# Kernel optimization log

Measured on AMD Instinct MI355X. Metric: run time of the kernel, lower is better.

Reference implementation:

```python
import jax, jax.numpy as jnp
import numpy as np

B, S, E, H, D = 16, 1024, 768, 12, 64  # batch, seq, n_embd, n_head, head_dim
F = 4 * E
EPS = 1e-5


def layernorm(x, g, b):
    mu = jnp.mean(x, axis=-1, keepdims=True)
    var = jnp.mean((x - mu) ** 2, axis=-1, keepdims=True)
    return (x - mu) * jax.lax.rsqrt(var + EPS) * g + b


def setup_inputs() -> dict:
    key = jax.random.key(0)
    ks = jax.random.split(key, 12)
    w = lambda k, shape: jax.random.normal(k, shape, dtype=jnp.float32) * 0.02
    return {
        "x": jax.random.normal(ks[0], (B, S, E), dtype=jnp.float32),
        # per-head q/k/v projections stacked over heads: [H, E, D]
        "Wq": w(ks[1], (H, E, D)), "bq": jnp.zeros((H, D), jnp.float32),
        "Wk": w(ks[2], (H, E, D)), "bk": jnp.zeros((H, D), jnp.float32),
        "Wv": w(ks[3], (H, E, D)), "bv": jnp.zeros((H, D), jnp.float32),
        "Wp": w(ks[4], (E, E)), "bp": jnp.zeros((E,), jnp.float32),
        "ln1_g": jnp.ones((E,), jnp.float32), "ln1_b": jnp.zeros((E,), jnp.float32),
        "ln2_g": jnp.ones((E,), jnp.float32), "ln2_b": jnp.zeros((E,), jnp.float32),
        "W1": w(ks[5], (E, F)), "b1": jnp.zeros((F,), jnp.float32),
        "W2": w(ks[6], (F, E)), "b2": jnp.zeros((E,), jnp.float32),
        "lnf_g": jnp.ones((E,), jnp.float32), "lnf_b": jnp.zeros((E,), jnp.float32),
    }


def reference(x, Wq, bq, Wk, bk, Wv, bv, Wp, bp,
              ln1_g, ln1_b, ln2_g, ln2_b, W1, b1, W2, b2, lnf_g, lnf_b):
    # --- multi-head causal attention (batched over heads, same math as the
    # per-head loop in the original) ---
    h = layernorm(x, ln1_g, ln1_b)
    q = jnp.einsum('bse,hed->bhsd', h, Wq) + bq[None, :, None, :]
    k = jnp.einsum('bse,hed->bhsd', h, Wk) + bk[None, :, None, :]
    v = jnp.einsum('bse,hed->bhsd', h, Wv) + bv[None, :, None, :]
    scores = jnp.einsum('bhsd,bhtd->bhst', q, k)
    causal = jnp.tril(jnp.ones((S, S), dtype=bool))
    # original: mask with -inf, then divide by sqrt(head_dim), then softmax
    scores = jnp.where(causal, scores, -jnp.inf) / np.sqrt(D).astype(np.float32)
    attn = jax.nn.softmax(scores, axis=-1)
    o = jnp.einsum('bhst,bhtd->bhsd', attn, v)
    o = o.transpose(0, 2, 1, 3).reshape(B, S, E)  # concat heads
    x = x + (o @ Wp + bp)
    # --- FFN with post-net LayerNorm (as in the original FeedForward) ---
    h2 = layernorm(x, ln2_g, ln2_b)
    f = jax.nn.gelu(h2 @ W1 + b1, approximate=False) @ W2 + b2
    f = layernorm(f, lnf_g, lnf_b)
    return x + f
```

## Files before the change

kernel.cpp:

```cpp
#include <hip/hip_runtime.h>
#include <math.h>

typedef unsigned short u16;
typedef __attribute__((ext_vector_type(8))) short s16x8;
typedef __attribute__((ext_vector_type(4))) float f32x4;

#define NB 16
#define NS 1024
#define NE 768
#define NH 12
#define ND 64
#define NF 3072
#define NBS (NB*NS)
#define NBH (NB*NH)

__device__ __forceinline__ u16 f2bf(float f){
  unsigned u = __float_as_uint(f);
  unsigned r = (u + 0x7fffu + ((u >> 16) & 1u)) >> 16;
  return (u16)r;
}

__device__ __forceinline__ void gload16(const void* g, void* l){
  __builtin_amdgcn_global_load_lds((const __attribute__((address_space(1))) void*)g,
                                   (__attribute__((address_space(3))) void*)l, 16, 0, 0);
}

__global__ __launch_bounds__(256) void pack_t(const float* __restrict__ W,
                                              u16* __restrict__ Wt, int N, int K){
  __shared__ u16 tile[64*72];
  const int tid = threadIdx.x;
  const int n0 = blockIdx.x*64, k0 = blockIdx.y*64;
  #pragma unroll
  for (int it = 0; it < 4; ++it){
    int c = it*256 + tid;
    int row = c >> 4, col = (c & 15) * 4;
    float4 v = *(const float4*)(W + (size_t)(k0+row)*N + n0 + col);
    tile[row*72+col+0] = f2bf(v.x); tile[row*72+col+1] = f2bf(v.y);
    tile[row*72+col+2] = f2bf(v.z); tile[row*72+col+3] = f2bf(v.w);
  }
  __syncthreads();
  #pragma unroll
  for (int it = 0; it < 2; ++it){
    int c = it*256 + tid;
    int nr = c >> 3, kc = (c & 7) * 8;
    s16x8 val;
    #pragma unroll
    for (int j = 0; j < 8; ++j) val[j] = tile[(kc+j)*72 + nr];
    *(s16x8*)(Wt + (size_t)(n0+nr)*K + k0 + kc) = val;
  }
}

__global__ __launch_bounds__(256) void pack_qkv(const float* __restrict__ Wq,
    const float* __restrict__ Wk, const float* __restrict__ Wv,
    const float* __restrict__ bq, const float* __restrict__ bk,
    const float* __restrict__ bv, u16* __restrict__ Wt, float* __restrict__ bias){
  __shared__ u16 tile[64*72];
  const int tid = threadIdx.x;
  const int n0 = blockIdx.x*64, e0 = blockIdx.y*64;
  const int p = n0 / NE, rr = n0 % NE, h = rr >> 6;
  const float* Wsrc = (p==0) ? Wq : ((p==1) ? Wk : Wv);
  #pragma unroll
  for (int it = 0; it < 4; ++it){
    int c = it*256 + tid;
    int row = c >> 4, col = (c & 15) * 4;
    float4 v = *(const float4*)(Wsrc + ((size_t)h*NE + e0 + row)*ND + col);
    tile[row*72+col+0] = f2bf(v.x); tile[row*72+col+1] = f2bf(v.y);
    tile[row*72+col+2] = f2bf(v.z); tile[row*72+col+3] = f2bf(v.w);
  }
  __syncthreads();
  #pragma unroll
  for (int it = 0; it < 2; ++it){
    int c = it*256 + tid;
    int dr = c >> 3, ec = (c & 7) * 8;
    s16x8 val;
    #pragma unroll
    for (int j = 0; j < 8; ++j) val[j] = tile[(ec+j)*72 + dr];
    *(s16x8*)(Wt + (size_t)(n0+dr)*NE + e0 + ec) = val;
  }
  if (e0 == 0 && tid < 64){
    const float* bsrc = (p==0) ? bq : ((p==1) ? bk : bv);
    bias[n0 + tid] = bsrc[rr + tid];
  }
}

__global__ __launch_bounds__(256) void ln_bf16(const float* __restrict__ x,
    const float* __restrict__ g, const float* __restrict__ b, u16* __restrict__ out){
  __shared__ float red[4];
  const int row = blockIdx.x, tid = threadIdx.x;
  const float* xr = x + (size_t)row*NE;
  float v0 = xr[tid], v1 = xr[tid+256], v2 = xr[tid+512];
  float s = v0 + v1 + v2;
  #pragma unroll
  for (int off = 32; off > 0; off >>= 1) s += __shfl_down(s, off);
  if ((tid & 63) == 0) red[tid >> 6] = s;
  __syncthreads();
  float mu = (red[0]+red[1]+red[2]+red[3]) * (1.f/NE);
  float d0 = v0-mu, d1 = v1-mu, d2 = v2-mu;
  float q = d0*d0 + d1*d1 + d2*d2;
  #pragma unroll
  for (int off = 32; off > 0; off >>= 1) q += __shfl_down(q, off);
  __syncthreads();
  if ((tid & 63) == 0) red[tid >> 6] = q;
  __syncthreads();
  float rs = rsqrtf((red[0]+red[1]+red[2]+red[3]) * (1.f/NE) + 1e-5f);
  u16* orow = out + (size_t)row*NE;
  orow[tid]     = f2bf(d0*rs*g[tid]     + b[tid]);
  orow[tid+256] = f2bf(d1*rs*g[tid+256] + b[tid+256]);
  orow[tid+512] = f2bf(d2*rs*g[tid+512] + b[tid+512]);
}

__global__ __launch_bounds__(256) void ln_add_out(const float* __restrict__ f2,
    const float* __restrict__ g, const float* __restrict__ b, float* __restrict__ x1){
  __shared__ float red[4];
  const int row = blockIdx.x, tid = threadIdx.x;
  const float* xr = f2 + (size_t)row*NE;
  float v0 = xr[tid], v1 = xr[tid+256], v2 = xr[tid+512];
  float s = v0 + v1 + v2;
  #pragma unroll
  for (int off = 32; off > 0; off >>= 1) s += __shfl_down(s, off);
  if ((tid & 63) == 0) red[tid >> 6] = s;
  __syncthreads();
  float mu = (red[0]+red[1]+red[2]+red[3]) * (1.f/NE);
  float d0 = v0-mu, d1 = v1-mu, d2 = v2-mu;
  float q = d0*d0 + d1*d1 + d2*d2;
  #pragma unroll
  for (int off = 32; off > 0; off >>= 1) q += __shfl_down(q, off);
  __syncthreads();
  if ((tid & 63) == 0) red[tid >> 6] = q;
  __syncthreads();
  float rs = rsqrtf((red[0]+red[1]+red[2]+red[3]) * (1.f/NE) + 1e-5f);
  float* orow = x1 + (size_t)row*NE;
  orow[tid]     += d0*rs*g[tid]     + b[tid];
  orow[tid+256] += d1*rs*g[tid+256] + b[tid+256];
  orow[tid+512] += d2*rs*g[tid+512] + b[tid+512];
}

template<int EPI>
__global__ __launch_bounds__(256, 2)
void gemm_bt(const u16* __restrict__ A, const u16* __restrict__ Bt,
             const float* __restrict__ bias, const float* __restrict__ resid,
             float* __restrict__ outF, u16* __restrict__ outU,
             u16* __restrict__ oq, u16* __restrict__ ok, u16* __restrict__ ov,
             int M, int N, int K)
{
  __shared__ u16 As[128*32];
  __shared__ u16 Bs[128*32];
  const int tid = threadIdx.x;
  const int lane = tid & 63, wv = tid >> 6;
  const int wm = wv >> 1, wn = wv & 1;
  const int r = lane & 15, g4 = lane >> 4;
  const int m0 = blockIdx.y*128, n0 = blockIdx.x*128;

  f32x4 acc[4][4] = {};

  for (int kt = 0; kt < K; kt += 32) {
    __syncthreads();
    #pragma unroll
    for (int it = 0; it < 2; ++it) {
      int c = it*256 + tid;
      int row = c >> 2, kc = (c & 3) << 3;
      gload16(A  + (size_t)(m0+row)*K + kt + kc, As + (size_t)(it*256 + wv*64)*8);
      gload16(Bt + (size_t)(n0+row)*K + kt + kc, Bs + (size_t)(it*256 + wv*64)*8);
    }
    __syncthreads();
    s16x8 aF[4], bF[4];
    #pragma unroll
    for (int mi = 0; mi < 4; ++mi)
      aF[mi] = *(const s16x8*)(As + (wm*64 + mi*16 + r)*32 + g4*8);
    #pragma unroll
    for (int ni = 0; ni < 4; ++ni)
      bF[ni] = *(const s16x8*)(Bs + (wn*64 + ni*16 + r)*32 + g4*8);
    #pragma unroll
    for (int mi = 0; mi < 4; ++mi)
      #pragma unroll
      for (int ni = 0; ni < 4; ++ni)
        acc[mi][ni] = __builtin_amdgcn_mfma_f32_16x16x32_bf16(aF[mi], bF[ni], acc[mi][ni], 0, 0, 0);
  }

  const int colb = n0 + wn*64, rowb = m0 + wm*64;
  #pragma unroll
  for (int mi = 0; mi < 4; ++mi) {
    #pragma unroll
    for (int ni = 0; ni < 4; ++ni) {
      const int col = colb + ni*16 + r;
      const float bv = bias[col];
      #pragma unroll
      for (int i = 0; i < 4; ++i) {
        const int row = rowb + mi*16 + g4*4 + i;
        float v = acc[mi][ni][i] + bv;
        if (EPI == 0) {
          int p = col / NE, rr2 = col % NE;
          int hh = rr2 >> 6, d = rr2 & 63;
          int bb = row >> 10, ss = row & (NS-1);
          size_t idx = (((size_t)(bb*NH + hh))*NS + ss)*ND + d;
          if (p == 1) v *= 0.18033688011112042f;
          u16 val = f2bf(v);
          if (p == 0) oq[idx] = val;
          else if (p == 1) ok[idx] = val;
          else ov[idx] = val;
        } else if (EPI == 1) {
          size_t idx = (size_t)row*NE + col;
          outF[idx] = resid[idx] + v;
        } else if (EPI == 2) {
          float ge = 0.5f * v * (1.0f + erff(v * 0.70710678118654752f));
          outU[(size_t)row*NF + col] = f2bf(ge);
        } else {
          outF[(size_t)row*NE + col] = v;
        }
      }
    }
  }
}

__global__ __launch_bounds__(256) void transpose_v(const u16* __restrict__ v,
                                                   u16* __restrict__ vT){
  __shared__ u16 tile[64*80];
  const int tid = threadIdx.x;
  const int t0 = blockIdx.x*64, bh = blockIdx.y;
  const u16* src = v + ((size_t)bh*NS + t0)*ND;
  #pragma unroll
  for (int it = 0; it < 2; ++it){
    int c = it*256 + tid;
    int row = c >> 3, col = (c & 7) * 8;
    *(s16x8*)(tile + row*80 + col) = *(const s16x8*)(src + (size_t)row*ND + col);
  }
  __syncthreads();
  u16* dst = vT + (size_t)bh*ND*NS + t0;
  #pragma unroll
  for (int it = 0; it < 2; ++it){
    int c = it*256 + tid;
    int d = c >> 3, tc = (c & 7) * 8;
    s16x8 val;
    #pragma unroll
    for (int j = 0; j < 8; ++j) val[j] = tile[(tc+j)*80 + d];
    *(s16x8*)(dst + (size_t)d*NS + tc) = val;
  }
}

__global__ __launch_bounds__(256, 2)
void attn(const u16* __restrict__ q, const u16* __restrict__ k,
          const u16* __restrict__ vT, u16* __restrict__ o)
{
  __shared__ u16 Ks[64*80];
  __shared__ u16 Vs[64*80];
  __shared__ u16 Ps[64*80];
  const int tid = threadIdx.x, lane = tid & 63, w = tid >> 6;
  const int r = lane & 15, g4 = lane >> 4;
  const int phys = blockIdx.y * 8 + blockIdx.x;
  const int logical = (phys & 7) * 192 + (phys >> 3);
  const int bh = logical >> 3, qt = logical & 7;
  const int bb = bh / NH, hh = bh % NH;
  const int rgb0 = qt * 64, rgb1 = (15 - qt) * 64;

  s16x8 qf[2][2];
  {
    const u16* qb = q + ((size_t)bh*NS + w*16 + r)*ND;
    qf[0][0] = *(const s16x8*)(qb + (size_t)rgb0*ND + g4*8);
    qf[0][1] = *(const s16x8*)(qb + (size_t)rgb0*ND + 32 + g4*8);
    qf[1][0] = *(const s16x8*)(qb + (size_t)rgb1*ND + g4*8);
    qf[1][1] = *(const s16x8*)(qb + (size_t)rgb1*ND + 32 + g4*8);
  }

  f32x4 oacc[2][4] = {};
  float mrow[2][4], lrow[2][4];
  #pragma unroll
  for (int rg = 0; rg < 2; ++rg)
    #pragma unroll
    for (int i = 0; i < 4; ++i){ mrow[rg][i] = -INFINITY; lrow[rg][i] = 0.f; }

  const u16* kbase = k  + (size_t)bh*NS*ND;
  const u16* vbase = vT + (size_t)bh*ND*NS;
  const int nt = 16 - qt;

  for (int t = 0; t < nt; ++t) {
    const int kt0 = t*64;
    __syncthreads();
    #pragma unroll
    for (int it = 0; it < 2; ++it) {
      int c = it*256 + tid;
      int rowi = c >> 3, coli = (c & 7) * 8;
      *(s16x8*)(Ks + rowi*80 + coli) = *(const s16x8*)(kbase + (size_t)(kt0+rowi)*ND + coli);
      *(s16x8*)(Vs + rowi*80 + coli) = *(const s16x8*)(vbase + (size_t)rowi*NS + kt0 + coli);
    }
    __syncthreads();

    #pragma unroll
    for (int rg = 0; rg < 2; ++rg) {
      const int rgb = (rg == 0) ? rgb0 : rgb1;
      if (kt0 > rgb) continue;

      f32x4 sc[4];
      __builtin_amdgcn_s_setprio(1);
      #pragma unroll
      for (int ni = 0; ni < 4; ++ni) {
        s16x8 kf0 = *(const s16x8*)(Ks + (ni*16+r)*80 + g4*8);
        s16x8 kf1 = *(const s16x8*)(Ks + (ni*16+r)*80 + 32 + g4*8);
        f32x4 tacc = {};
        tacc = __builtin_amdgcn_mfma_f32_16x16x32_bf16(qf[rg][0], kf0, tacc, 0, 0, 0);
        tacc = __builtin_amdgcn_mfma_f32_16x16x32_bf16(qf[rg][1], kf1, tacc, 0, 0, 0);
        sc[ni] = tacc;
      }
      __builtin_amdgcn_s_setprio(0);

      float mx[4];
      #pragma unroll
      for (int i = 0; i < 4; ++i) mx[i] = mrow[rg][i];
      if (kt0 == rgb) {
        #pragma unroll
        for (int ni = 0; ni < 4; ++ni)
          #pragma unroll
          for (int i = 0; i < 4; ++i) {
            if (ni*16 + r > w*16 + g4*4 + i) sc[ni][i] = -INFINITY;
            mx[i] = fmaxf(mx[i], sc[ni][i]);
          }
      } else {
        #pragma unroll
        for (int ni = 0; ni < 4; ++ni)
          #pragma unroll
          for (int i = 0; i < 4; ++i) mx[i] = fmaxf(mx[i], sc[ni][i]);
      }
      #pragma unroll
      for (int i = 0; i < 4; ++i) {
        #pragma unroll
        for (int off = 1; off < 16; off <<= 1) mx[i] = fmaxf(mx[i], __shfl_xor(mx[i], off));
      }
      bool nogrow = true;
      #pragma unroll
      for (int i = 0; i < 4; ++i) nogrow = nogrow && (mx[i] - mrow[rg][i] <= 8.f);
      float psum[4];
      if (!__all(nogrow)) {
        #pragma unroll
        for (int i = 0; i < 4; ++i) {
          float corr = exp2f(mrow[rg][i] - mx[i]);
          mrow[rg][i] = mx[i];
          lrow[rg][i] *= corr;
          #pragma unroll
          for (int di = 0; di < 4; ++di) oacc[rg][di][i] *= corr;
        }
      }
      #pragma unroll
      for (int ni = 0; ni < 4; ++ni)
        #pragma unroll
        for (int i = 0; i < 4; ++i) {
          float p = exp2f(sc[ni][i] - mrow[rg][i]);
          if (ni == 0) psum[i] = p; else psum[i] += p;
          Ps[(w*16 + g4*4 + i)*80 + ni*16 + r] = f2bf(p);
        }
      #pragma unroll
      for (int i = 0; i < 4; ++i) {
        #pragma unroll
        for (int off = 1; off < 16; off <<= 1) psum[i] += __shfl_xor(psum[i], off);
        lrow[rg][i] += psum[i];
      }
      __builtin_amdgcn_s_setprio(1);
      #pragma unroll
      for (int kk = 0; kk < 2; ++kk) {
        s16x8 pf = *(const s16x8*)(&Ps[(w*16 + r)*80 + kk*32 + g4*8]);
        #pragma unroll
        for (int di = 0; di < 4; ++di) {
          s16x8 vf = *(const s16x8*)(&Vs[(di*16+r)*80 + kk*32 + g4*8]);
          oacc[rg][di] = __builtin_amdgcn_mfma_f32_16x16x32_bf16(pf, vf, oacc[rg][di], 0, 0, 0);
        }
      }
      __builtin_amdgcn_s_setprio(0);
    }
  }

  #pragma unroll
  for (int rg = 0; rg < 2; ++rg) {
    const int rgb = (rg == 0) ? rgb0 : rgb1;
    #pragma unroll
    for (int i = 0; i < 4; ++i) {
      float inv = 1.f / lrow[rg][i];
      int s = rgb + w*16 + g4*4 + i;
      u16* orow = o + ((size_t)(bb*NS + s))*NE + hh*ND;
      #pragma unroll
      for (int di = 0; di < 4; ++di)
        orow[di*16 + r] = f2bf(oacc[rg][di][i] * inv);
    }
  }
}

extern "C" void kernel_launch(void* const* d_in, const int* in_sizes, int n_in,
                              void* d_out, int out_size, void* d_ws, size_t ws_size,
                              hipStream_t stream)
{
  const float* x   = (const float*)d_in[0];
  const float* Wq  = (const float*)d_in[1];
  const float* bq  = (const float*)d_in[2];
  const float* Wk  = (const float*)d_in[3];
  const float* bk  = (const float*)d_in[4];
  const float* Wv  = (const float*)d_in[5];
  const float* bv  = (const float*)d_in[6];
  const float* Wp  = (const float*)d_in[7];
  const float* bp  = (const float*)d_in[8];
  const float* g1  = (const float*)d_in[9];
  const float* b1n = (const float*)d_in[10];
  const float* g2  = (const float*)d_in[11];
  const float* b2n = (const float*)d_in[12];
  const float* W1  = (const float*)d_in[13];
  const float* b1f = (const float*)d_in[14];
  const float* W2  = (const float*)d_in[15];
  const float* b2f = (const float*)d_in[16];
  const float* gf  = (const float*)d_in[17];
  const float* bf  = (const float*)d_in[18];

  char* ws = (char*)d_ws;
  u16*   WqkvT = (u16*)(ws + 0);
  u16*   WpT   = (u16*)(ws + 3538944);
  u16*   W1T   = (u16*)(ws + 4718592);
  u16*   W2T   = (u16*)(ws + 9437184);
  float* qkvb  = (float*)(ws + 14155776);
  u16*   hbuf  = (u16*)(ws + 14164992);
  u16*   qbuf  = (u16*)(ws + 39330816);
  u16*   kbuf  = (u16*)(ws + 64496640);
  u16*   vbuf  = (u16*)(ws + 89662464);
  u16*   vTbuf = (u16*)(ws + 114828288);
  const size_t base_end = 139994112;
  float* f2    = (float*)kbuf;
  float* x1    = (float*)d_out;

  const size_t f1_full = (size_t)NBS * NF * 2;
  u16* f1buf;
  int mc;
  if (ws_size >= base_end + f1_full) {
    f1buf = (u16*)(ws + base_end);
    mc = NBS;
  } else {
    f1buf = vbuf;
    size_t cap = (ws_size < base_end ? ws_size : base_end) - 89662464;
    mc = (int)(cap / ((size_t)NF * 2)) / 128 * 128;
    if (mc <= 0) mc = 128;
    if (mc > NBS) mc = NBS;
  }

  pack_qkv<<<dim3(36, 12), 256, 0, stream>>>(Wq, Wk, Wv, bq, bk, bv, WqkvT, qkvb);
  pack_t  <<<dim3(NE/64, NE/64), 256, 0, stream>>>(Wp, WpT, NE, NE);
  pack_t  <<<dim3(NF/64, NE/64), 256, 0, stream>>>(W1, W1T, NF, NE);
  pack_t  <<<dim3(NE/64, NF/64), 256, 0, stream>>>(W2, W2T, NE, NF);

  ln_bf16<<<NBS, 256, 0, stream>>>(x, g1, b1n, hbuf);
  gemm_bt<0><<<dim3(2304/128, NBS/128), 256, 0, stream>>>(hbuf, WqkvT, qkvb, nullptr,
      nullptr, nullptr, qbuf, kbuf, vbuf, NBS, 2304, NE);
  transpose_v<<<dim3(NS/64, NBH), 256, 0, stream>>>(vbuf, vTbuf);
  attn<<<dim3(8, NBH), 256, 0, stream>>>(qbuf, kbuf, vTbuf, hbuf);
  gemm_bt<1><<<dim3(NE/128, NBS/128), 256, 0, stream>>>(hbuf, WpT, bp, x,
      x1, nullptr, nullptr, nullptr, nullptr, NBS, NE, NE);
  ln_bf16<<<NBS, 256, 0, stream>>>(x1, g2, b2n, qbuf);
  for (int r0 = 0; r0 < NBS; r0 += mc) {
    int m = (NBS - r0 < mc) ? (NBS - r0) : mc;
    gemm_bt<2><<<dim3(NF/128, m/128), 256, 0, stream>>>(qbuf + (size_t)r0*NE, W1T, b1f,
        nullptr, nullptr, f1buf, nullptr, nullptr, nullptr, m, NF, NE);
    gemm_bt<3><<<dim3(NE/128, m/128), 256, 0, stream>>>(f1buf, W2T, b2f, nullptr,
        f2 + (size_t)r0*NE, nullptr, nullptr, nullptr, nullptr, m, NE, NF);
  }
  ln_add_out<<<NBS, 256, 0, stream>>>(f2, gf, bf, x1);
}
```

Measured before the change: 655.5 us.

## Replace 128x128 GEMM with double-buffered 256x256 tile, 512-thread kernel

Replaces the 128x128x32 bf16 MFMA GEMM with a 256x256x64 tile kernel run by 512 threads (8 waves, each owning a 128x64 sub-tile). Shared-memory buffers are double-buffered, so the global-to-LDS loads for the next K step are issued before computing the current one. MFMA issue is wrapped in raised wave priority. The aim is more operand reuse per LDS byte and hiding global-load latency. The cost is about 128KB of LDS per block and far fewer blocks for the N=768 GEMMs, which can underfill the CUs. The unswizzled 128-byte LDS row stride may also cause bank conflicts.

```diff
diff --git a/kernel.cpp b/kernel.cpp
--- a/kernel.cpp
+++ b/kernel.cpp
@@ -136,50 +136,74 @@
 }
 
 template<int EPI>
-__global__ __launch_bounds__(256, 2)
-void gemm_bt(const u16* __restrict__ A, const u16* __restrict__ Bt,
+__global__ __launch_bounds__(512, 2)
+void gemm256(const u16* __restrict__ A, const u16* __restrict__ Bt,
              const float* __restrict__ bias, const float* __restrict__ resid,
              float* __restrict__ outF, u16* __restrict__ outU,
              u16* __restrict__ oq, u16* __restrict__ ok, u16* __restrict__ ov,
              int M, int N, int K)
 {
-  __shared__ u16 As[128*32];
-  __shared__ u16 Bs[128*32];
+  __shared__ u16 As[2][256*64];
+  __shared__ u16 Bs[2][256*64];
   const int tid = threadIdx.x;
-  const int lane = tid & 63, wv = tid >> 6;
-  const int wm = wv >> 1, wn = wv & 1;
+  const int lane = tid & 63, wid = tid >> 6;
+  const int wm = wid >> 2, wn = wid & 3;
   const int r = lane & 15, g4 = lane >> 4;
-  const int m0 = blockIdx.y*128, n0 = blockIdx.x*128;
-
-  f32x4 acc[4][4] = {};
-
-  for (int kt = 0; kt < K; kt += 32) {
-    __syncthreads();
-    #pragma unroll
-    for (int it = 0; it < 2; ++it) {
-      int c = it*256 + tid;
-      int row = c >> 2, kc = (c & 3) << 3;
-      gload16(A  + (size_t)(m0+row)*K + kt + kc, As + (size_t)(it*256 + wv*64)*8);
-      gload16(Bt + (size_t)(n0+row)*K + kt + kc, Bs + (size_t)(it*256 + wv*64)*8);
-    }
-    __syncthreads();
-    s16x8 aF[4], bF[4];
-    #pragma unroll
-    for (int mi = 0; mi < 4; ++mi)
-      aF[mi] = *(const s16x8*)(As + (wm*64 + mi*16 + r)*32 + g4*8);
-    #pragma unroll
-    for (int ni = 0; ni < 4; ++ni)
-      bF[ni] = *(const s16x8*)(Bs + (wn*64 + ni*16 + r)*32 + g4*8);
-    #pragma unroll
-    for (int mi = 0; mi < 4; ++mi)
-      #pragma unroll
-      for (int ni = 0; ni < 4; ++ni)
-        acc[mi][ni] = __builtin_amdgcn_mfma_f32_16x16x32_bf16(aF[mi], bF[ni], acc[mi][ni], 0, 0, 0);
-  }
-
-  const int colb = n0 + wn*64, rowb = m0 + wm*64;
-  #pragma unroll
-  for (int mi = 0; mi < 4; ++mi) {
+  const int m0 = blockIdx.y*256, n0 = blockIdx.x*256;
+  const int srow = tid >> 3, scol = (tid & 7) * 8;
+
+  f32x4 acc[8][4] = {};
+  const int nk = K >> 6;
+
+  #pragma unroll
+  for (int i = 0; i < 4; ++i) {
+    gload16(A  + (size_t)(m0 + i*64 + srow)*K + scol, &As[0][i*4096 + wid*512]);
+    gload16(Bt + (size_t)(n0 + i*64 + srow)*K + scol, &Bs[0][i*4096 + wid*512]);
+  }
+
+  for (int t = 0; t < nk; ++t) {
+    const int cb = t & 1;
+    asm volatile("s_waitcnt vmcnt(0)" ::: "memory");
+    __builtin_amdgcn_s_barrier();
+    __builtin_amdgcn_sched_barrier(0);
+    if (t+1 < nk) {
+      const int ktn = (t+1) << 6;
+      #pragma unroll
+      for (int i = 0; i < 4; ++i) {
+        gload16(A  + (size_t)(m0 + i*64 + srow)*K + ktn + scol, &As[cb^1][i*4096 + wid*512]);
+        gload16(Bt + (size_t)(n0 + i*64 + srow)*K + ktn + scol, &Bs[cb^1][i*4096 + wid*512]);
+      }
+    }
+    #pragma unroll
+    for (int q = 0; q < 4; ++q) {
+      const int mih = (q >> 1) * 4, nih = (q & 1) * 2;
+      s16x8 aF[4][2], bF[2][2];
+      #pragma unroll
+      for (int mi = 0; mi < 4; ++mi)
+        #pragma unroll
+        for (int kk = 0; kk < 2; ++kk)
+          aF[mi][kk] = *(const s16x8*)(&As[cb][(wm*128 + (mih+mi)*16 + r)*64 + kk*32 + g4*8]);
+      #pragma unroll
+      for (int ni = 0; ni < 2; ++ni)
+        #pragma unroll
+        for (int kk = 0; kk < 2; ++kk)
+          bF[ni][kk] = *(const s16x8*)(&Bs[cb][(wn*64 + (nih+ni)*16 + r)*64 + kk*32 + g4*8]);
+      __builtin_amdgcn_s_setprio(1);
+      #pragma unroll
+      for (int mi = 0; mi < 4; ++mi)
+        #pragma unroll
+        for (int ni = 0; ni < 2; ++ni)
+          #pragma unroll
+          for (int kk = 0; kk < 2; ++kk)
+            acc[mih+mi][nih+ni] = __builtin_amdgcn_mfma_f32_16x16x32_bf16(
+                aF[mi][kk], bF[ni][kk], acc[mih+mi][nih+ni], 0, 0, 0);
+      __builtin_amdgcn_s_setprio(0);
+    }
+  }
+
+  const int colb = n0 + wn*64, rowb = m0 + wm*128;
+  #pragma unroll
+  for (int mi = 0; mi < 8; ++mi) {
     #pragma unroll
     for (int ni = 0; ni < 4; ++ni) {
       const int col = colb + ni*16 + r;
@@ -429,8 +453,8 @@
   } else {
     f1buf = vbuf;
     size_t cap = (ws_size < base_end ? ws_size : base_end) - 89662464;
-    mc = (int)(cap / ((size_t)NF * 2)) / 128 * 128;
-    if (mc <= 0) mc = 128;
+    mc = (int)(cap / ((size_t)NF * 2)) / 256 * 256;
+    if (mc <= 0) mc = 256;
     if (mc > NBS) mc = NBS;
   }
 
@@ -440,18 +464,18 @@
   pack_t  <<<dim3(NE/64, NF/64), 256, 0, stream>>>(W2, W2T, NE, NF);
 
   ln_bf16<<<NBS, 256, 0, stream>>>(x, g1, b1n, hbuf);
-  gemm_bt<0><<<dim3(2304/128, NBS/128), 256, 0, stream>>>(hbuf, WqkvT, qkvb, nullptr,
+  gemm256<0><<<dim3(2304/256, NBS/256), 512, 0, stream>>>(hbuf, WqkvT, qkvb, nullptr,
       nullptr, nullptr, qbuf, kbuf, vbuf, NBS, 2304, NE);
   transpose_v<<<dim3(NS/64, NBH), 256, 0, stream>>>(vbuf, vTbuf);
   attn<<<dim3(8, NBH), 256, 0, stream>>>(qbuf, kbuf, vTbuf, hbuf);
-  gemm_bt<1><<<dim3(NE/128, NBS/128), 256, 0, stream>>>(hbuf, WpT, bp, x,
+  gemm256<1><<<dim3(NE/256, NBS/256), 512, 0, stream>>>(hbuf, WpT, bp, x,
       x1, nullptr, nullptr, nullptr, nullptr, NBS, NE, NE);
   ln_bf16<<<NBS, 256, 0, stream>>>(x1, g2, b2n, qbuf);
   for (int r0 = 0; r0 < NBS; r0 += mc) {
     int m = (NBS - r0 < mc) ? (NBS - r0) : mc;
-    gemm_bt<2><<<dim3(NF/128, m/128), 256, 0, stream>>>(qbuf + (size_t)r0*NE, W1T, b1f,
+    gemm256<2><<<dim3(NF/256, m/256), 512, 0, stream>>>(qbuf + (size_t)r0*NE, W1T, b1f,
         nullptr, nullptr, f1buf, nullptr, nullptr, nullptr, m, NF, NE);
-    gemm_bt<3><<<dim3(NE/128, m/128), 256, 0, stream>>>(f1buf, W2T, b2f, nullptr,
+    gemm256<3><<<dim3(NE/256, m/256), 512, 0, stream>>>(f1buf, W2T, b2f, nullptr,
         f2 + (size_t)r0*NE, nullptr, nullptr, nullptr, nullptr, m, NE, NF);
   }
   ln_add_out<<<NBS, 256, 0, stream>>>(f2, gf, bf, x1);
```

After: 886.9 us. 35.3% more time.
